# Kernel optimization log

Measured on AMD Instinct MI355X. Metric: run time of the kernel, lower is better.

The kernel has to match this reference:

```python
import jax, jax.numpy as jnp
import numpy as np

B, S, H = 4, 8192, 768
NH, HD = 12, 64          # num_heads, head_size
M = 64                   # projection_dim = min(256, HD)
EPS = 1e-6

def setup_inputs() -> dict:
    key = jax.random.key(0)
    ks = jax.random.split(key, 10)
    scale_w = 0.02
    scale_p = 1.0 / np.sqrt(HD)
    return {
        'hidden_states': jax.random.normal(ks[0], (B, S, H), jnp.float32),
        'Wq': jax.random.normal(ks[1], (H, H), jnp.float32) * scale_w,
        'bq': jnp.zeros((H,), jnp.float32),
        'Wk': jax.random.normal(ks[2], (H, H), jnp.float32) * scale_w,
        'bk': jnp.zeros((H,), jnp.float32),
        'Wv': jax.random.normal(ks[3], (H, H), jnp.float32) * scale_w,
        'bv': jnp.zeros((H,), jnp.float32),
        'Wo': jax.random.normal(ks[4], (H, H), jnp.float32) * scale_w,
        'bo': jnp.zeros((H,), jnp.float32),
        'projection_matrix': jax.random.normal(ks[5], (NH, HD, M), jnp.float32) * scale_p,
    }

def reference(hidden_states, Wq, bq, Wk, bk, Wv, bv, Wo, bo, projection_matrix):
    b, s, h = hidden_states.shape
    def heads(x):  # [b,s,h] -> [b,nh,s,hd]
        return x.reshape(b, s, NH, HD).transpose(0, 2, 1, 3)
    q = heads(hidden_states @ Wq + bq)
    k = heads(hidden_states @ Wk + bk)
    v = heads(hidden_states @ Wv + bv)
    # random-feature projection + stabilized exp feature map
    qp = jnp.einsum('bhnd,hdm->bhnm', q, projection_matrix)
    kp = jnp.einsum('bhnd,hdm->bhnm', k, projection_matrix)
    qp = jnp.exp(qp - jnp.max(qp, axis=-1, keepdims=True))
    kp = jnp.exp(kp - jnp.max(kp, axis=-1, keepdims=True))
    # O(n) linear attention: kv summary [b,h,m,hd]
    kv = jnp.einsum('bhnm,bhnd->bhmd', kp, v)
    qkv = jnp.einsum('bhnm,bhmd->bhnd', qp, kv)
    k_sum = jnp.sum(kp, axis=2)                      # [b,h,m]
    normalizer = jnp.einsum('bhnm,bhm->bhn', qp, k_sum)[..., None]
    ctx = qkv / (normalizer + EPS)
    ctx = ctx.transpose(0, 2, 1, 3).reshape(b, s, NH * HD)
    return ctx @ Wo + bo
```

## Files before the change

### kernel.cpp

```cpp
#include <hip/hip_runtime.h>
#include <hip/hip_bf16.h>


#define S_    8192
#define H_    768
#define NH_   12
#define EPS_  1e-6f

typedef unsigned short U16;
typedef short bf16x8 __attribute__((ext_vector_type(8)));
typedef float f32x4  __attribute__((ext_vector_type(4)));

__device__ __forceinline__ U16 f2b(float x) {
  unsigned u = __float_as_uint(x);
  return (U16)((u + 0x7fffu + ((u >> 16) & 1u)) >> 16);
}
__device__ __forceinline__ float b2f(U16 h) {
  return __uint_as_float(((unsigned)h) << 16);
}
__device__ __forceinline__ void gl2lds16(const void* g, void* l) {
  __builtin_amdgcn_global_load_lds(
      (const __attribute__((address_space(1))) void*)g,
      (__attribute__((address_space(3))) void*)l, 16, 0, 0);
}

__global__ void zero_f32(float* __restrict__ p, int n) {
  int i = blockIdx.x * 256 + threadIdx.x;
  if (i < n) p[i] = 0.f;
}

__global__ void cvt_f32_bf16(const float* __restrict__ src, U16* __restrict__ hi, int n4) {
  int i = blockIdx.x * 256 + threadIdx.x;
  if (i >= n4) return;
  float4 x = ((const float4*)src)[i];
  ushort4 h;
  h.x = f2b(x.x); h.y = f2b(x.y); h.z = f2b(x.z); h.w = f2b(x.w);
  ((ushort4*)hi)[i] = h;
}

__global__ void fold_proj(const float* __restrict__ Wq, const float* __restrict__ bq,
                          const float* __restrict__ Wk, const float* __restrict__ bk,
                          const float* __restrict__ P,
                          float* __restrict__ Wqp, float* __restrict__ bqp,
                          float* __restrict__ Wkp, float* __restrict__ bkp) {
  __shared__ float Pl[64 * 64];
  __shared__ float WL[4 * 64];
  int h = blockIdx.y, kc = blockIdx.x, tid = threadIdx.x;
  const float* W  = blockIdx.z ? Wk : Wq;
  const float* bb = blockIdx.z ? bk : bq;
  float* Wout = blockIdx.z ? Wkp : Wqp;
  float* bout = blockIdx.z ? bkp : bqp;
  const float4* P4 = (const float4*)(P + (size_t)h * 4096);
#pragma unroll
  for (int i = 0; i < 4; ++i) ((float4*)Pl)[tid + i * 256] = P4[tid + i * 256];
  WL[tid] = W[(size_t)(kc * 4 + (tid >> 6)) * H_ + h * 64 + (tid & 63)];
  __syncthreads();
  int kl = tid >> 6, m = tid & 63;
  float acc = 0.f;
#pragma unroll
  for (int d = 0; d < 64; ++d) acc += WL[kl * 64 + d] * Pl[d * 64 + m];
  Wout[(size_t)(kc * 4 + kl) * H_ + h * 64 + m] = acc;
  if (kc == 0 && tid < 64) {
    float a2 = 0.f;
    for (int d = 0; d < 64; ++d) a2 += bb[h * 64 + d] * Pl[d * 64 + tid];
    bout[h * 64 + tid] = a2;
  }
}

__global__ void build_cat(const float* __restrict__ Wqp, const float* __restrict__ Wkp,
                          const float* __restrict__ Wv,  const float* __restrict__ Wo,
                          U16* __restrict__ WcatH, U16* __restrict__ WoTH) {
  int k = blockIdx.x * 256 + threadIdx.x;
  int r = blockIdx.y;
  float v; U16* dh; size_t off;
  if (r < 768)       { v = Wqp[(size_t)k * H_ + r];          off = (size_t)r * H_ + k;          dh = WcatH; }
  else if (r < 1536) { v = Wkp[(size_t)k * H_ + (r - 768)];  off = (size_t)r * H_ + k;          dh = WcatH; }
  else if (r < 2304) { v = Wv [(size_t)k * H_ + (r - 1536)]; off = (size_t)r * H_ + k;          dh = WcatH; }
  else               { v = Wo [(size_t)k * H_ + (r - 2304)]; off = (size_t)(r - 2304) * H_ + k; dh = WoTH; }
  dh[off] = f2b(v);
}

__global__ void build_bias(const float* __restrict__ bqp, const float* __restrict__ bkp,
                           const float* __restrict__ bv, float* __restrict__ biasC) {
  int i = blockIdx.x * 256 + threadIdx.x;
  if (i >= 2304) return;
  biasC[i] = i < 768 ? bqp[i] : (i < 1536 ? bkp[i - 768] : bv[i - 1536]);
}

__global__ __launch_bounds__(256, 4) void gemm_qkv(
    const U16* __restrict__ Ahi, const U16* __restrict__ Bhi,
    const float* __restrict__ bias,
    U16* __restrict__ qp, U16* __restrict__ kpT, U16* __restrict__ vT) {
  __shared__ __align__(16) U16 Us[2 * 128 * 32];
  const int tid = threadIdx.x, w = tid >> 6, lane = tid & 63;
  const int quad = lane >> 4, l16 = lane & 15;
  const int rowA0 = blockIdx.y * 128, colB0 = blockIdx.x * 128;
  const int wm = w & 1, wn = w >> 1;
  const int K = 768;
  f32x4 acc[4][4] = {};
  const U16* srcs[4];
  unsigned ldsoff[4];
#pragma unroll
  for (int t = 0; t < 4; ++t) {
    int c = w * 4 + t, cc = c & 7, buf = c >> 3;
    const U16* base = buf ? Bhi : Ahi;
    int r0 = buf ? colB0 : rowA0;
    srcs[t] = base + (size_t)(r0 + cc * 16 + (lane >> 2)) * K + (lane & 3) * 8;
    ldsoff[t] = c * 512;
  }
  for (int k0 = 0; k0 < K; k0 += 32) {
#pragma unroll
    for (int t = 0; t < 4; ++t) gl2lds16(srcs[t] + k0, &Us[ldsoff[t]]);
    __syncthreads();
    bf16x8 ah[4];
#pragma unroll
    for (int i = 0; i < 4; ++i)
      ah[i] = *(const bf16x8*)&Us[(wm * 64 + i * 16 + l16) * 32 + quad * 8];
#pragma unroll
    for (int j = 0; j < 4; ++j) {
      bf16x8 bh = *(const bf16x8*)&Us[4096 + (wn * 64 + j * 16 + l16) * 32 + quad * 8];
#pragma unroll
      for (int i = 0; i < 4; ++i)
        acc[i][j] = __builtin_amdgcn_mfma_f32_16x16x32_bf16(ah[i], bh, acc[i][j], 0, 0, 0);
    }
    __syncthreads();
  }
  const int col64 = colB0 + wn * 64;
  float bj[4];
#pragma unroll
  for (int j = 0; j < 4; ++j) bj[j] = bias[col64 + j * 16 + l16];
  if (col64 < 768) {
    const int h = col64 >> 6;
#pragma unroll
    for (int i = 0; i < 4; ++i) {
#pragma unroll
      for (int r = 0; r < 4; ++r) {
        int row = rowA0 + wm * 64 + i * 16 + quad * 4 + r;
        float v0 = acc[i][0][r] + bj[0], v1 = acc[i][1][r] + bj[1];
        float v2 = acc[i][2][r] + bj[2], v3 = acc[i][3][r] + bj[3];
        float mx = fmaxf(fmaxf(v0, v1), fmaxf(v2, v3));
        mx = fmaxf(mx, __shfl_xor(mx, 1));
        mx = fmaxf(mx, __shfl_xor(mx, 2));
        mx = fmaxf(mx, __shfl_xor(mx, 4));
        mx = fmaxf(mx, __shfl_xor(mx, 8));
        int b = row >> 13, s = row & 8191;
        size_t base = ((size_t)(b * NH_ + h) * S_ + s) * 64 + l16;
        qp[base +  0] = f2b(__expf(v0 - mx));
        qp[base + 16] = f2b(__expf(v1 - mx));
        qp[base + 32] = f2b(__expf(v2 - mx));
        qp[base + 48] = f2b(__expf(v3 - mx));
      }
    }
  } else {
    const int isv = col64 >= 1536;
    const int h = (col64 - (isv ? 1536 : 768)) >> 6;
    U16* dstT = isv ? vT : kpT;
#pragma unroll
    for (int i = 0; i < 4; ++i) {
      float er[4][4];
#pragma unroll
      for (int r = 0; r < 4; ++r) {
        float v0 = acc[i][0][r] + bj[0], v1 = acc[i][1][r] + bj[1];
        float v2 = acc[i][2][r] + bj[2], v3 = acc[i][3][r] + bj[3];
        if (!isv) {
          float mx = fmaxf(fmaxf(v0, v1), fmaxf(v2, v3));
          mx = fmaxf(mx, __shfl_xor(mx, 1));
          mx = fmaxf(mx, __shfl_xor(mx, 2));
          mx = fmaxf(mx, __shfl_xor(mx, 4));
          mx = fmaxf(mx, __shfl_xor(mx, 8));
          v0 = __expf(v0 - mx); v1 = __expf(v1 - mx);
          v2 = __expf(v2 - mx); v3 = __expf(v3 - mx);
        }
        er[0][r] = v0; er[1][r] = v1; er[2][r] = v2; er[3][r] = v3;
      }
      int n = rowA0 + wm * 64 + i * 16 + quad * 4;
      int b = n >> 13, s = n & 8191;
      int bh = b * NH_ + h;
#pragma unroll
      for (int j = 0; j < 4; ++j) {
        ushort4 o;
        o.x = f2b(er[j][0]); o.y = f2b(er[j][1]);
        o.z = f2b(er[j][2]); o.w = f2b(er[j][3]);
        *(ushort4*)&dstT[((size_t)bh * 64 + j * 16 + l16) * S_ + s] = o;
      }
    }
  }
}

__global__ __launch_bounds__(256, 4) void kv_accum_mfma(
    const U16* __restrict__ kpT, const U16* __restrict__ vT,
    float* __restrict__ kvT) {
  __shared__ __align__(16) U16 Us[2 * 64 * 64];
  const int tid = threadIdx.x, w = tid >> 6, lane = tid & 63;
  const int quad = lane >> 4, l16 = lane & 15;
  const int bh = blockIdx.y;
  const int n0 = blockIdx.x * 1024;
  const U16* srcs[4];
  unsigned ldsoff[4];
#pragma unroll
  for (int t = 0; t < 4; ++t) {
    int c = w * 4 + t, buf = c >> 3;
    int r = (c & 7) * 8 + (lane >> 3);
    const U16* base = buf ? kpT : vT;
    srcs[t] = base + ((size_t)bh * 64 + r) * S_ + n0 + (lane & 7) * 8;
    ldsoff[t] = buf * 4096 + (c & 7) * 512;
  }
  f32x4 acc[4] = {};
  float ks[4] = {0.f, 0.f, 0.f, 0.f};
  for (int nc = 0; nc < 1024; nc += 64) {
#pragma unroll
    for (int t = 0; t < 4; ++t) gl2lds16(srcs[t] + nc, &Us[ldsoff[t]]);
    __syncthreads();
#pragma unroll
    for (int k0 = 0; k0 < 64; k0 += 32) {
      bf16x8 av = *(const bf16x8*)&Us[(w * 16 + l16) * 64 + k0 + quad * 8];
#pragma unroll
      for (int j = 0; j < 4; ++j) {
        bf16x8 bk = *(const bf16x8*)&Us[4096 + (j * 16 + l16) * 64 + k0 + quad * 8];
        if (w == 0) {
#pragma unroll
          for (int e = 0; e < 8; ++e) ks[j] += b2f((U16)bk[e]);
        }
        acc[j] = __builtin_amdgcn_mfma_f32_16x16x32_bf16(av, bk, acc[j], 0, 0, 0);
      }
    }
    __syncthreads();
  }
#pragma unroll
  for (int j = 0; j < 4; ++j)
#pragma unroll
    for (int r = 0; r < 4; ++r) {
      int d = w * 16 + quad * 4 + r;
      atomicAdd(&kvT[((size_t)bh * 80 + d) * 64 + j * 16 + l16], acc[j][r]);
    }
  if (w == 0) {
#pragma unroll
    for (int j = 0; j < 4; ++j) {
      ks[j] += __shfl_xor(ks[j], 16);
      ks[j] += __shfl_xor(ks[j], 32);
    }
    if (lane < 16) {
#pragma unroll
      for (int j = 0; j < 4; ++j)
        atomicAdd(&kvT[((size_t)bh * 80 + 64) * 64 + j * 16 + lane], ks[j]);
    }
  }
}

__global__ __launch_bounds__(256) void ctx_gemm_k(
    const U16* __restrict__ qp, const float* __restrict__ kvT,
    U16* __restrict__ ctx) {
  __shared__ __align__(16) U16 As[128 * 64];
  __shared__ __align__(16) U16 Bs[80 * 64];
  int bh = blockIdx.y, row0 = blockIdx.x * 128;
  int tid = threadIdx.x, w = tid >> 6, lane = tid & 63;
  int quad = lane >> 4, l16 = lane & 15;
  const U16* Ab = qp + ((size_t)bh * S_ + row0) * 64;
#pragma unroll
  for (int t = 0; t < 4; ++t) {
    int cb = (w * 4 + t) * 64;
    gl2lds16(Ab + (size_t)(cb + lane) * 8, &As[cb * 8]);
  }
  const float4* kv4 = (const float4*)(kvT + (size_t)bh * 5120);
#pragma unroll
  for (int t = 0; t < 5; ++t) {
    int idx = t * 256 + tid;
    float4 f = kv4[idx];
    ushort4 o;
    o.x = f2b(f.x); o.y = f2b(f.y); o.z = f2b(f.z); o.w = f2b(f.w);
    *(ushort4*)&Bs[idx * 4] = o;
  }
  __syncthreads();
  f32x4 acc[2][5] = {};
#pragma unroll
  for (int k0 = 0; k0 < 64; k0 += 32) {
    bf16x8 a[2], fb[5];
#pragma unroll
    for (int i = 0; i < 2; ++i)
      a[i] = *(const bf16x8*)&As[(w * 32 + i * 16 + l16) * 64 + k0 + quad * 8];
#pragma unroll
    for (int j = 0; j < 5; ++j)
      fb[j] = *(const bf16x8*)&Bs[(j * 16 + l16) * 64 + k0 + quad * 8];
#pragma unroll
    for (int j = 0; j < 5; ++j)
#pragma unroll
      for (int i = 0; i < 2; ++i)
        acc[i][j] = __builtin_amdgcn_mfma_f32_16x16x32_bf16(a[i], fb[j], acc[i][j], 0, 0, 0);
  }
  int b = bh / NH_, h = bh - b * NH_;
#pragma unroll
  for (int i = 0; i < 2; ++i) {
#pragma unroll
    for (int r = 0; r < 4; ++r) {
      int s = row0 + w * 32 + i * 16 + quad * 4 + r;
      float nv = __shfl(acc[i][4][r], lane & 48);
      float inv = 1.f / (nv + EPS_);
      size_t base = ((size_t)b * S_ + s) * H_ + h * 64;
#pragma unroll
      for (int j = 0; j < 4; ++j)
        ctx[base + j * 16 + l16] = f2b(acc[i][j][r] * inv);
    }
  }
}

__global__ __launch_bounds__(256, 4) void gemm_out(
    const U16* __restrict__ Ahi, const U16* __restrict__ Bhi,
    const float* __restrict__ bias, float* __restrict__ C, int K, int ldc) {
  __shared__ __align__(16) U16 Us[2 * 128 * 32];
  const int tid = threadIdx.x, w = tid >> 6, lane = tid & 63;
  const int quad = lane >> 4, l16 = lane & 15;
  const int rowA0 = blockIdx.y * 128, colB0 = blockIdx.x * 128;
  const int wm = w & 1, wn = w >> 1;
  f32x4 acc[4][4] = {};
  const U16* srcs[4];
  unsigned ldsoff[4];
#pragma unroll
  for (int t = 0; t < 4; ++t) {
    int c = w * 4 + t, cc = c & 7, buf = c >> 3;
    const U16* base = buf ? Bhi : Ahi;
    int r0 = buf ? colB0 : rowA0;
    srcs[t] = base + (size_t)(r0 + cc * 16 + (lane >> 2)) * K + (lane & 3) * 8;
    ldsoff[t] = c * 512;
  }
  for (int k0 = 0; k0 < K; k0 += 32) {
#pragma unroll
    for (int t = 0; t < 4; ++t) gl2lds16(srcs[t] + k0, &Us[ldsoff[t]]);
    __syncthreads();
    bf16x8 ah[4];
#pragma unroll
    for (int i = 0; i < 4; ++i)
      ah[i] = *(const bf16x8*)&Us[(wm * 64 + i * 16 + l16) * 32 + quad * 8];
#pragma unroll
    for (int j = 0; j < 4; ++j) {
      bf16x8 bh = *(const bf16x8*)&Us[4096 + (wn * 64 + j * 16 + l16) * 32 + quad * 8];
#pragma unroll
      for (int i = 0; i < 4; ++i)
        acc[i][j] = __builtin_amdgcn_mfma_f32_16x16x32_bf16(ah[i], bh, acc[i][j], 0, 0, 0);
    }
    __syncthreads();
  }
#pragma unroll
  for (int i = 0; i < 4; ++i) {
    int row = rowA0 + wm * 64 + i * 16 + quad * 4;
#pragma unroll
    for (int j = 0; j < 4; ++j) {
      int col = colB0 + wn * 64 + j * 16 + l16;
      float bvv = bias[col];
#pragma unroll
      for (int r = 0; r < 4; ++r)
        C[(size_t)(row + r) * ldc + col] = acc[i][j][r] + bvv;
    }
  }
}

extern "C" void kernel_launch(void* const* d_in, const int* in_sizes, int n_in,
                              void* d_out, int out_size, void* d_ws, size_t ws_size,
                              hipStream_t stream) {
  const float* hs = (const float*)d_in[0];
  const float* Wq = (const float*)d_in[1];
  const float* bq = (const float*)d_in[2];
  const float* Wk = (const float*)d_in[3];
  const float* bk = (const float*)d_in[4];
  const float* Wv = (const float*)d_in[5];
  const float* bv = (const float*)d_in[6];
  const float* Wo = (const float*)d_in[7];
  const float* bo = (const float*)d_in[8];
  const float* P  = (const float*)d_in[9];
  float* out = (float*)d_out;

  char* ws = (char*)d_ws;
  size_t off = 0;
  auto alloc = [&](size_t bytes) -> void* {
    void* p = ws + off;
    off = (off + bytes + 255) & ~(size_t)255;
    return p;
  };
  U16*   hs_hi = (U16*)alloc(50331648);
  float* WqpF  = (float*)alloc(2359296);
  float* WkpF  = (float*)alloc(2359296);
  float* bqpF  = (float*)alloc(3072);
  float* bkpF  = (float*)alloc(3072);
  U16*   WcatH = (U16*)alloc(3538944);
  U16*   WoTH  = (U16*)alloc(1179648);
  float* biasC = (float*)alloc(9216);
  U16*   qp    = (U16*)alloc(50331648);
  U16*   kpT   = (U16*)alloc(50331648);
  U16*   vT    = (U16*)alloc(50331648);
  float* kvT   = (float*)alloc(983040);
  U16*   ctx   = hs_hi;

  zero_f32<<<dim3(960), dim3(256), 0, stream>>>(kvT, 245760);
  cvt_f32_bf16<<<dim3(24576), dim3(256), 0, stream>>>(hs, hs_hi, 6291456);
  fold_proj<<<dim3(192, 12, 2), dim3(256), 0, stream>>>(Wq, bq, Wk, bk, P, WqpF, bqpF, WkpF, bkpF);
  build_cat<<<dim3(3, 3072), dim3(256), 0, stream>>>(WqpF, WkpF, Wv, Wo, WcatH, WoTH);
  build_bias<<<dim3(9), dim3(256), 0, stream>>>(bqpF, bkpF, bv, biasC);
  gemm_qkv<<<dim3(18, 256), dim3(256), 0, stream>>>(hs_hi, WcatH, biasC, qp, kpT, vT);
  kv_accum_mfma<<<dim3(8, 48), dim3(256), 0, stream>>>(kpT, vT, kvT);
  ctx_gemm_k<<<dim3(64, 48), dim3(256), 0, stream>>>(qp, kvT, ctx);
  gemm_out<<<dim3(6, 256), dim3(256), 0, stream>>>(ctx, WoTH, bo, out, 768, 768);
}
```

Baseline: 504.2 us.

## Persistent pipelined QKV GEMM and fused ctx-output kernel with swizzled LDS

The QKV GEMM becomes a persistent-style kernel: each block keeps one 128-row A strip and loops over nine column tiles, with BK=64, double-buffered async global-to-LDS staging, an XOR-swizzled LDS layout and raised priority around the MFMA section. The ctx computation and the output projection are fused into one kernel. It builds a 64x768 ctx tile in LDS from qp and a bf16 copy of kv, then multiplies it by Wo with double-buffered staging, so the ctx round trip through global memory and one launch are gone. kv_accum splits the sequence into more blocks and a small conversion kernel turns kv into bf16. The large LDS footprint (about 132KB) and lower occupancy risk latency exposure, and the fused kernel recomputes the per-head ctx inside each block.

```diff
diff --git a/kernel.cpp b/kernel.cpp
--- a/kernel.cpp
+++ b/kernel.cpp
@@ -87,101 +87,146 @@
   biasC[i] = i < 768 ? bqp[i] : (i < 1536 ? bkp[i - 768] : bv[i - 1536]);
 }
 
-__global__ __launch_bounds__(256, 4) void gemm_qkv(
+__global__ __launch_bounds__(256, 2) void gemm_qkv(
     const U16* __restrict__ Ahi, const U16* __restrict__ Bhi,
     const float* __restrict__ bias,
     U16* __restrict__ qp, U16* __restrict__ kpT, U16* __restrict__ vT) {
-  __shared__ __align__(16) U16 Us[2 * 128 * 32];
+  __shared__ __align__(16) U16 Us[32768];
   const int tid = threadIdx.x, w = tid >> 6, lane = tid & 63;
   const int quad = lane >> 4, l16 = lane & 15;
-  const int rowA0 = blockIdx.y * 128, colB0 = blockIdx.x * 128;
+  const int b = blockIdx.x;
+  const int mt = b & 255, nt0 = b >> 8;
+  const int rowA0 = mt * 128;
   const int wm = w & 1, wn = w >> 1;
-  const int K = 768;
-  f32x4 acc[4][4] = {};
-  const U16* srcs[4];
-  unsigned ldsoff[4];
+  const U16* srcA[4];
+  int rowBl[4];
+  unsigned ldsc[4];
+  const int kch = ((lane & 7) ^ (lane >> 3)) * 8;
 #pragma unroll
   for (int t = 0; t < 4; ++t) {
-    int c = w * 4 + t, cc = c & 7, buf = c >> 3;
-    const U16* base = buf ? Bhi : Ahi;
-    int r0 = buf ? colB0 : rowA0;
-    srcs[t] = base + (size_t)(r0 + cc * 16 + (lane >> 2)) * K + (lane & 3) * 8;
-    ldsoff[t] = c * 512;
-  }
-  for (int k0 = 0; k0 < K; k0 += 32) {
-#pragma unroll
-    for (int t = 0; t < 4; ++t) gl2lds16(srcs[t] + k0, &Us[ldsoff[t]]);
-    __syncthreads();
-    bf16x8 ah[4];
-#pragma unroll
-    for (int i = 0; i < 4; ++i)
-      ah[i] = *(const bf16x8*)&Us[(wm * 64 + i * 16 + l16) * 32 + quad * 8];
-#pragma unroll
-    for (int j = 0; j < 4; ++j) {
-      bf16x8 bh = *(const bf16x8*)&Us[4096 + (wn * 64 + j * 16 + l16) * 32 + quad * 8];
+    int c = w * 4 + t;
+    int row = c * 8 + (lane >> 3);
+    srcA[t] = Ahi + (size_t)(rowA0 + row) * H_ + kch;
+    rowBl[t] = row;
+    ldsc[t] = (unsigned)c * 512;
+  }
+  auto stage = [&](int jn, int tn, int bi) {
+    const int colB = (nt0 + 2 * jn) * 128;
+    unsigned ub = (unsigned)bi * 16384u;
+#pragma unroll
+    for (int t = 0; t < 4; ++t) {
+      gl2lds16(srcA[t] + tn * 64, &Us[ub + ldsc[t]]);
+      gl2lds16(Bhi + (size_t)(colB + rowBl[t]) * H_ + tn * 64 + kch,
+               &Us[ub + 8192u + ldsc[t]]);
+    }
+  };
+
+  stage(0, 0, 0);
+  for (int jj = 0; jj < 9; ++jj) {
+    const int colB0 = (nt0 + 2 * jj) * 128;
+    f32x4 acc[4][4] = {};
+    for (int t = 0; t < 12; ++t) {
+      const bool more = !(jj == 8 && t == 11);
+      if (more) {
+        if (t < 11) stage(jj, t + 1, (t + 1) & 1);
+        else        stage(jj + 1, 0, 0);
+        asm volatile("s_waitcnt vmcnt(8)" ::: "memory");
+      } else {
+        asm volatile("s_waitcnt vmcnt(0)" ::: "memory");
+      }
+      __builtin_amdgcn_sched_barrier(0);
+      __builtin_amdgcn_s_barrier();
+      __builtin_amdgcn_sched_barrier(0);
+      const unsigned ab = (unsigned)(t & 1) * 16384u;
+      bf16x8 ah[4][2], bh[4][2];
 #pragma unroll
       for (int i = 0; i < 4; ++i)
-        acc[i][j] = __builtin_amdgcn_mfma_f32_16x16x32_bf16(ah[i], bh, acc[i][j], 0, 0, 0);
-    }
-    __syncthreads();
-  }
-  const int col64 = colB0 + wn * 64;
-  float bj[4];
-#pragma unroll
-  for (int j = 0; j < 4; ++j) bj[j] = bias[col64 + j * 16 + l16];
-  if (col64 < 768) {
-    const int h = col64 >> 6;
-#pragma unroll
-    for (int i = 0; i < 4; ++i) {
-#pragma unroll
-      for (int r = 0; r < 4; ++r) {
-        int row = rowA0 + wm * 64 + i * 16 + quad * 4 + r;
-        float v0 = acc[i][0][r] + bj[0], v1 = acc[i][1][r] + bj[1];
-        float v2 = acc[i][2][r] + bj[2], v3 = acc[i][3][r] + bj[3];
-        float mx = fmaxf(fmaxf(v0, v1), fmaxf(v2, v3));
-        mx = fmaxf(mx, __shfl_xor(mx, 1));
-        mx = fmaxf(mx, __shfl_xor(mx, 2));
-        mx = fmaxf(mx, __shfl_xor(mx, 4));
-        mx = fmaxf(mx, __shfl_xor(mx, 8));
-        int b = row >> 13, s = row & 8191;
-        size_t base = ((size_t)(b * NH_ + h) * S_ + s) * 64 + l16;
-        qp[base +  0] = f2b(__expf(v0 - mx));
-        qp[base + 16] = f2b(__expf(v1 - mx));
-        qp[base + 32] = f2b(__expf(v2 - mx));
-        qp[base + 48] = f2b(__expf(v3 - mx));
-      }
-    }
-  } else {
-    const int isv = col64 >= 1536;
-    const int h = (col64 - (isv ? 1536 : 768)) >> 6;
-    U16* dstT = isv ? vT : kpT;
-#pragma unroll
-    for (int i = 0; i < 4; ++i) {
-      float er[4][4];
-#pragma unroll
-      for (int r = 0; r < 4; ++r) {
-        float v0 = acc[i][0][r] + bj[0], v1 = acc[i][1][r] + bj[1];
-        float v2 = acc[i][2][r] + bj[2], v3 = acc[i][3][r] + bj[3];
-        if (!isv) {
+#pragma unroll
+        for (int ks = 0; ks < 2; ++ks)
+          ah[i][ks] = *(const bf16x8*)&Us[ab +
+              (unsigned)((wm * 64 + i * 16 + l16) * 64 +
+                         (((ks * 4 + quad) ^ (l16 & 7)) * 8))];
+#pragma unroll
+      for (int j = 0; j < 4; ++j)
+#pragma unroll
+        for (int ks = 0; ks < 2; ++ks)
+          bh[j][ks] = *(const bf16x8*)&Us[ab + 8192u +
+              (unsigned)((wn * 64 + j * 16 + l16) * 64 +
+                         (((ks * 4 + quad) ^ (l16 & 7)) * 8))];
+      asm volatile("s_waitcnt lgkmcnt(0)" ::: "memory");
+      __builtin_amdgcn_sched_barrier(0);
+      __builtin_amdgcn_s_setprio(1);
+#pragma unroll
+      for (int ks = 0; ks < 2; ++ks)
+#pragma unroll
+        for (int j = 0; j < 4; ++j)
+#pragma unroll
+          for (int i = 0; i < 4; ++i)
+            acc[i][j] = __builtin_amdgcn_mfma_f32_16x16x32_bf16(
+                ah[i][ks], bh[j][ks], acc[i][j], 0, 0, 0);
+      __builtin_amdgcn_s_setprio(0);
+      __builtin_amdgcn_sched_barrier(0);
+      __builtin_amdgcn_s_barrier();
+      __builtin_amdgcn_sched_barrier(0);
+    }
+    const int col64 = colB0 + wn * 64;
+    float bj[4];
+#pragma unroll
+    for (int j = 0; j < 4; ++j) bj[j] = bias[col64 + j * 16 + l16];
+    if (col64 < 768) {
+      const int h = col64 >> 6;
+#pragma unroll
+      for (int i = 0; i < 4; ++i) {
+#pragma unroll
+        for (int r = 0; r < 4; ++r) {
+          int row = rowA0 + wm * 64 + i * 16 + quad * 4 + r;
+          float v0 = acc[i][0][r] + bj[0], v1 = acc[i][1][r] + bj[1];
+          float v2 = acc[i][2][r] + bj[2], v3 = acc[i][3][r] + bj[3];
           float mx = fmaxf(fmaxf(v0, v1), fmaxf(v2, v3));
           mx = fmaxf(mx, __shfl_xor(mx, 1));
           mx = fmaxf(mx, __shfl_xor(mx, 2));
           mx = fmaxf(mx, __shfl_xor(mx, 4));
           mx = fmaxf(mx, __shfl_xor(mx, 8));
-          v0 = __expf(v0 - mx); v1 = __expf(v1 - mx);
-          v2 = __expf(v2 - mx); v3 = __expf(v3 - mx);
+          int bb = row >> 13, s = row & 8191;
+          size_t base = ((size_t)(bb * NH_ + h) * S_ + s) * 64 + l16;
+          qp[base +  0] = f2b(__expf(v0 - mx));
+          qp[base + 16] = f2b(__expf(v1 - mx));
+          qp[base + 32] = f2b(__expf(v2 - mx));
+          qp[base + 48] = f2b(__expf(v3 - mx));
         }
-        er[0][r] = v0; er[1][r] = v1; er[2][r] = v2; er[3][r] = v3;
-      }
-      int n = rowA0 + wm * 64 + i * 16 + quad * 4;
-      int b = n >> 13, s = n & 8191;
-      int bh = b * NH_ + h;
-#pragma unroll
-      for (int j = 0; j < 4; ++j) {
-        ushort4 o;
-        o.x = f2b(er[j][0]); o.y = f2b(er[j][1]);
-        o.z = f2b(er[j][2]); o.w = f2b(er[j][3]);
-        *(ushort4*)&dstT[((size_t)bh * 64 + j * 16 + l16) * S_ + s] = o;
+      }
+    } else {
+      const int isv = col64 >= 1536;
+      const int h = (col64 - (isv ? 1536 : 768)) >> 6;
+      U16* dstT = isv ? vT : kpT;
+#pragma unroll
+      for (int i = 0; i < 4; ++i) {
+        float er[4][4];
+#pragma unroll
+        for (int r = 0; r < 4; ++r) {
+          float v0 = acc[i][0][r] + bj[0], v1 = acc[i][1][r] + bj[1];
+          float v2 = acc[i][2][r] + bj[2], v3 = acc[i][3][r] + bj[3];
+          if (!isv) {
+            float mx = fmaxf(fmaxf(v0, v1), fmaxf(v2, v3));
+            mx = fmaxf(mx, __shfl_xor(mx, 1));
+            mx = fmaxf(mx, __shfl_xor(mx, 2));
+            mx = fmaxf(mx, __shfl_xor(mx, 4));
+            mx = fmaxf(mx, __shfl_xor(mx, 8));
+            v0 = __expf(v0 - mx); v1 = __expf(v1 - mx);
+            v2 = __expf(v2 - mx); v3 = __expf(v3 - mx);
+          }
+          er[0][r] = v0; er[1][r] = v1; er[2][r] = v2; er[3][r] = v3;
+        }
+        int n = rowA0 + wm * 64 + i * 16 + quad * 4;
+        int bb = n >> 13, s = n & 8191;
+        int bh2 = bb * NH_ + h;
+#pragma unroll
+        for (int j = 0; j < 4; ++j) {
+          ushort4 o;
+          o.x = f2b(er[j][0]); o.y = f2b(er[j][1]);
+          o.z = f2b(er[j][2]); o.w = f2b(er[j][3]);
+          *(ushort4*)&dstT[((size_t)bh2 * 64 + j * 16 + l16) * S_ + s] = o;
+        }
       }
     }
   }
@@ -194,7 +239,7 @@
   const int tid = threadIdx.x, w = tid >> 6, lane = tid & 63;
   const int quad = lane >> 4, l16 = lane & 15;
   const int bh = blockIdx.y;
-  const int n0 = blockIdx.x * 1024;
+  const int n0 = blockIdx.x * 512;
   const U16* srcs[4];
   unsigned ldsoff[4];
 #pragma unroll
@@ -207,7 +252,7 @@
   }
   f32x4 acc[4] = {};
   float ks[4] = {0.f, 0.f, 0.f, 0.f};
-  for (int nc = 0; nc < 1024; nc += 64) {
+  for (int nc = 0; nc < 512; nc += 64) {
 #pragma unroll
     for (int t = 0; t < 4; ++t) gl2lds16(srcs[t] + nc, &Us[ldsoff[t]]);
     __syncthreads();
@@ -247,108 +292,110 @@
   }
 }
 
-__global__ __launch_bounds__(256) void ctx_gemm_k(
-    const U16* __restrict__ qp, const float* __restrict__ kvT,
-    U16* __restrict__ ctx) {
-  __shared__ __align__(16) U16 As[128 * 64];
-  __shared__ __align__(16) U16 Bs[80 * 64];
-  int bh = blockIdx.y, row0 = blockIdx.x * 128;
-  int tid = threadIdx.x, w = tid >> 6, lane = tid & 63;
-  int quad = lane >> 4, l16 = lane & 15;
-  const U16* Ab = qp + ((size_t)bh * S_ + row0) * 64;
-#pragma unroll
-  for (int t = 0; t < 4; ++t) {
-    int cb = (w * 4 + t) * 64;
-    gl2lds16(Ab + (size_t)(cb + lane) * 8, &As[cb * 8]);
-  }
-  const float4* kv4 = (const float4*)(kvT + (size_t)bh * 5120);
-#pragma unroll
-  for (int t = 0; t < 5; ++t) {
-    int idx = t * 256 + tid;
-    float4 f = kv4[idx];
-    ushort4 o;
-    o.x = f2b(f.x); o.y = f2b(f.y); o.z = f2b(f.z); o.w = f2b(f.w);
-    *(ushort4*)&Bs[idx * 4] = o;
-  }
-  __syncthreads();
-  f32x4 acc[2][5] = {};
-#pragma unroll
-  for (int k0 = 0; k0 < 64; k0 += 32) {
-    bf16x8 a[2], fb[5];
-#pragma unroll
-    for (int i = 0; i < 2; ++i)
-      a[i] = *(const bf16x8*)&As[(w * 32 + i * 16 + l16) * 64 + k0 + quad * 8];
-#pragma unroll
-    for (int j = 0; j < 5; ++j)
-      fb[j] = *(const bf16x8*)&Bs[(j * 16 + l16) * 64 + k0 + quad * 8];
-#pragma unroll
-    for (int j = 0; j < 5; ++j)
-#pragma unroll
-      for (int i = 0; i < 2; ++i)
-        acc[i][j] = __builtin_amdgcn_mfma_f32_16x16x32_bf16(a[i], fb[j], acc[i][j], 0, 0, 0);
-  }
-  int b = bh / NH_, h = bh - b * NH_;
-#pragma unroll
-  for (int i = 0; i < 2; ++i) {
-#pragma unroll
-    for (int r = 0; r < 4; ++r) {
-      int s = row0 + w * 32 + i * 16 + quad * 4 + r;
-      float nv = __shfl(acc[i][4][r], lane & 48);
-      float inv = 1.f / (nv + EPS_);
-      size_t base = ((size_t)b * S_ + s) * H_ + h * 64;
-#pragma unroll
-      for (int j = 0; j < 4; ++j)
-        ctx[base + j * 16 + l16] = f2b(acc[i][j][r] * inv);
-    }
-  }
-}
-
-__global__ __launch_bounds__(256, 4) void gemm_out(
-    const U16* __restrict__ Ahi, const U16* __restrict__ Bhi,
-    const float* __restrict__ bias, float* __restrict__ C, int K, int ldc) {
-  __shared__ __align__(16) U16 Us[2 * 128 * 32];
+#define CTXP 776
+__global__ __launch_bounds__(256) void ctx_out(
+    const U16* __restrict__ qp, const U16* __restrict__ kvH,
+    const U16* __restrict__ WoTH, const float* __restrict__ bo,
+    float* __restrict__ out) {
+  extern __shared__ __align__(16) U16 smem[];
+  U16* ctxL = smem;
+  U16* WoTb = smem + 49664;
   const int tid = threadIdx.x, w = tid >> 6, lane = tid & 63;
   const int quad = lane >> 4, l16 = lane & 15;
-  const int rowA0 = blockIdx.y * 128, colB0 = blockIdx.x * 128;
+  const int row0 = blockIdx.x * 64;
+  const int bb = row0 >> 13, s0 = row0 & 8191;
+  const int bh0 = bb * NH_;
+#pragma unroll
+  for (int h = 0; h < 12; ++h) {
+    size_t qb = ((size_t)(bh0 + h) * S_ + s0 + w * 16 + l16) * 64;
+    bf16x8 a0 = *(const bf16x8*)&qp[qb + quad * 8];
+    bf16x8 a1 = *(const bf16x8*)&qp[qb + 32 + quad * 8];
+    const U16* kb = kvH + (size_t)(bh0 + h) * 5120;
+    f32x4 acc[5] = {};
+#pragma unroll
+    for (int j = 0; j < 5; ++j) {
+      bf16x8 b0 = *(const bf16x8*)&kb[(j * 16 + l16) * 64 + quad * 8];
+      bf16x8 b1 = *(const bf16x8*)&kb[(j * 16 + l16) * 64 + 32 + quad * 8];
+      acc[j] = __builtin_amdgcn_mfma_f32_16x16x32_bf16(a0, b0, acc[j], 0, 0, 0);
+      acc[j] = __builtin_amdgcn_mfma_f32_16x16x32_bf16(a1, b1, acc[j], 0, 0, 0);
+    }
+#pragma unroll
+    for (int r = 0; r < 4; ++r) {
+      float nv = __shfl(acc[4][r], lane & 48);
+      float inv = 1.f / (nv + EPS_);
+      int srow = w * 16 + quad * 4 + r;
+#pragma unroll
+      for (int j = 0; j < 4; ++j)
+        ctxL[srow * CTXP + h * 64 + j * 16 + l16] = f2b(acc[j][r] * inv);
+    }
+  }
+  __syncthreads();
   const int wm = w & 1, wn = w >> 1;
-  f32x4 acc[4][4] = {};
-  const U16* srcs[4];
-  unsigned ldsoff[4];
-#pragma unroll
-  for (int t = 0; t < 4; ++t) {
-    int c = w * 4 + t, cc = c & 7, buf = c >> 3;
-    const U16* base = buf ? Bhi : Ahi;
-    int r0 = buf ? colB0 : rowA0;
-    srcs[t] = base + (size_t)(r0 + cc * 16 + (lane >> 2)) * K + (lane & 3) * 8;
-    ldsoff[t] = c * 512;
-  }
-  for (int k0 = 0; k0 < K; k0 += 32) {
-#pragma unroll
-    for (int t = 0; t < 4; ++t) gl2lds16(srcs[t] + k0, &Us[ldsoff[t]]);
-    __syncthreads();
-    bf16x8 ah[4];
-#pragma unroll
-    for (int i = 0; i < 4; ++i)
-      ah[i] = *(const bf16x8*)&Us[(wm * 64 + i * 16 + l16) * 32 + quad * 8];
-#pragma unroll
-    for (int j = 0; j < 4; ++j) {
-      bf16x8 bh = *(const bf16x8*)&Us[4096 + (wn * 64 + j * 16 + l16) * 32 + quad * 8];
-#pragma unroll
-      for (int i = 0; i < 4; ++i)
-        acc[i][j] = __builtin_amdgcn_mfma_f32_16x16x32_bf16(ah[i], bh, acc[i][j], 0, 0, 0);
-    }
-    __syncthreads();
-  }
-#pragma unroll
-  for (int i = 0; i < 4; ++i) {
-    int row = rowA0 + wm * 64 + i * 16 + quad * 4;
-#pragma unroll
-    for (int j = 0; j < 4; ++j) {
-      int col = colB0 + wn * 64 + j * 16 + l16;
-      float bvv = bias[col];
-#pragma unroll
-      for (int r = 0; r < 4; ++r)
-        C[(size_t)(row + r) * ldc + col] = acc[i][j][r] + bvv;
+  const int kch = (((tid & 7) ^ ((tid >> 3) & 7)) * 8);
+  auto stageW = [&](int tt, int bi) {
+    int ntp = tt / 12, tp = tt - ntp * 12;
+    const U16* src = WoTH + (size_t)(ntp * 128 + (tid >> 3)) * H_ + tp * 64 + kch;
+    unsigned dst = (unsigned)bi * 8192u + (unsigned)tid * 8u;
+#pragma unroll
+    for (int k = 0; k < 4; ++k)
+      gl2lds16(src + (size_t)(32 * k) * H_, &WoTb[dst + (unsigned)k * 2048u]);
+  };
+  stageW(0, 0);
+  for (int nt = 0; nt < 6; ++nt) {
+    f32x4 acc2[2][4] = {};
+    for (int t = 0; t < 12; ++t) {
+      int tt = nt * 12 + t;
+      if (tt < 71) {
+        stageW(tt + 1, (tt + 1) & 1);
+        asm volatile("s_waitcnt vmcnt(4)" ::: "memory");
+      } else {
+        asm volatile("s_waitcnt vmcnt(0)" ::: "memory");
+      }
+      __builtin_amdgcn_sched_barrier(0);
+      __builtin_amdgcn_s_barrier();
+      __builtin_amdgcn_sched_barrier(0);
+      const unsigned ab = (unsigned)(tt & 1) * 8192u;
+      bf16x8 a2[2][2], b2[4][2];
+#pragma unroll
+      for (int i2 = 0; i2 < 2; ++i2)
+#pragma unroll
+        for (int ks = 0; ks < 2; ++ks)
+          a2[i2][ks] = *(const bf16x8*)&ctxL[
+              (wm * 32 + i2 * 16 + l16) * CTXP + t * 64 + ks * 32 + quad * 8];
+#pragma unroll
+      for (int j2 = 0; j2 < 4; ++j2)
+#pragma unroll
+        for (int ks = 0; ks < 2; ++ks)
+          b2[j2][ks] = *(const bf16x8*)&WoTb[ab +
+              (unsigned)((wn * 64 + j2 * 16 + l16) * 64 +
+                         (((ks * 4 + quad) ^ (l16 & 7)) * 8))];
+      asm volatile("s_waitcnt lgkmcnt(0)" ::: "memory");
+      __builtin_amdgcn_sched_barrier(0);
+      __builtin_amdgcn_s_setprio(1);
+#pragma unroll
+      for (int ks = 0; ks < 2; ++ks)
+#pragma unroll
+        for (int j2 = 0; j2 < 4; ++j2)
+#pragma unroll
+          for (int i2 = 0; i2 < 2; ++i2)
+            acc2[i2][j2] = __builtin_amdgcn_mfma_f32_16x16x32_bf16(
+                a2[i2][ks], b2[j2][ks], acc2[i2][j2], 0, 0, 0);
+      __builtin_amdgcn_s_setprio(0);
+      __builtin_amdgcn_sched_barrier(0);
+      __builtin_amdgcn_s_barrier();
+      __builtin_amdgcn_sched_barrier(0);
+    }
+#pragma unroll
+    for (int i2 = 0; i2 < 2; ++i2) {
+      int row = row0 + wm * 32 + i2 * 16 + quad * 4;
+#pragma unroll
+      for (int j2 = 0; j2 < 4; ++j2) {
+        int col = nt * 128 + wn * 64 + j2 * 16 + l16;
+        float bvv = bo[col];
+#pragma unroll
+        for (int r = 0; r < 4; ++r)
+          out[(size_t)(row + r) * H_ + col] = acc2[i2][j2][r] + bvv;
+      }
     }
   }
 }
@@ -387,15 +434,15 @@
   U16*   kpT   = (U16*)alloc(50331648);
   U16*   vT    = (U16*)alloc(50331648);
   float* kvT   = (float*)alloc(983040);
-  U16*   ctx   = hs_hi;
+  U16*   kvH   = (U16*)alloc(491520);
 
   zero_f32<<<dim3(960), dim3(256), 0, stream>>>(kvT, 245760);
   cvt_f32_bf16<<<dim3(24576), dim3(256), 0, stream>>>(hs, hs_hi, 6291456);
   fold_proj<<<dim3(192, 12, 2), dim3(256), 0, stream>>>(Wq, bq, Wk, bk, P, WqpF, bqpF, WkpF, bkpF);
   build_cat<<<dim3(3, 3072), dim3(256), 0, stream>>>(WqpF, WkpF, Wv, Wo, WcatH, WoTH);
   build_bias<<<dim3(9), dim3(256), 0, stream>>>(bqpF, bkpF, bv, biasC);
-  gemm_qkv<<<dim3(18, 256), dim3(256), 0, stream>>>(hs_hi, WcatH, biasC, qp, kpT, vT);
-  kv_accum_mfma<<<dim3(8, 48), dim3(256), 0, stream>>>(kpT, vT, kvT);
-  ctx_gemm_k<<<dim3(64, 48), dim3(256), 0, stream>>>(qp, kvT, ctx);
-  gemm_out<<<dim3(6, 256), dim3(256), 0, stream>>>(ctx, WoTH, bo, out, 768, 768);
-}
+  gemm_qkv<<<dim3(512), dim3(256), 0, stream>>>(hs_hi, WcatH, biasC, qp, kpT, vT);
+  kv_accum_mfma<<<dim3(16, 48), dim3(256), 0, stream>>>(kpT, vT, kvT);
+  cvt_f32_bf16<<<dim3(240), dim3(256), 0, stream>>>(kvT, kvH, 61440);
+  ctx_out<<<dim3(512), dim3(256), 132096, stream>>>(qp, kvH, WoTH, bo, out);
+}
```

New measurement: 499.2 us. Within noise of the previous version (-1.0%).
